# Optimization experiments

Hardware: AMD Instinct MI355X
Metric: run time of the kernel (lower is better)

The kernel has to match this reference:

```python
import jax, jax.numpy as jnp
import numpy as np

B, X, C = 8, 256, 256  # batch, feature axis, topfreq

def setup_inputs() -> dict:
    key = jax.random.key(0)
    k1, k2, k3, k4 = jax.random.split(key, 4)
    return {
        "amplitude": jax.random.normal(k1, (B, X, C), dtype=jnp.float32),
        "phase": jax.random.normal(k2, (B, X, C), dtype=jnp.float32),
        "A": jax.random.normal(k3, (C, C), dtype=jnp.float32),
        "w_amplitude": jnp.asarray(0.5, dtype=jnp.float32),
        "w_phase": jnp.asarray(0.5, dtype=jnp.float32),
        # uniform noise for gumbel sampling; keep away from 0 to avoid -log(-log(0))
        "gumbel_u": jax.random.uniform(k4, (B, C, C, 2), dtype=jnp.float32, minval=1e-6, maxval=1.0),
    }

def reference(amplitude, phase, A, w_amplitude, w_phase, gumbel_u):
    # pairwise diffs: (b, x, c, c)
    a_diff = amplitude[..., :, None] - amplitude[..., None, :]
    p_diff = phase[..., :, None] - phase[..., None, :]
    fused = w_amplitude * a_diff + w_phase * p_diff
    # einsum 'dd,bxcd->bxcd' == multiply by diag(A) along last dim
    temp = jnp.diagonal(A) * fused
    # einsum 'bxcd,bxcd->bcd' == sum of squares over x
    dist = jnp.sum(temp * temp, axis=1)  # (b, c, c)
    exp_dist = 1.0 / (dist + 1e-10)
    eye = jnp.eye(C, dtype=exp_dist.dtype)
    off_diag = 1.0 - eye
    exp_dist = exp_dist * off_diag
    exp_max = jax.lax.stop_gradient(jnp.max(exp_dist, axis=-1, keepdims=True))
    p = exp_dist / exp_max
    p = (p * off_diag + eye) * 0.99  # (b, c, c) in (0, 0.99]
    # bernoulli via 2-class gumbel-softmax (tau=1, hard, straight-through)
    logit = jnp.log(p / (1.0 - p))
    logits = jnp.stack([logit, -logit], axis=-1)  # (b, c, c, 2)
    g = -jnp.log(-jnp.log(gumbel_u))
    y = jax.nn.softmax(logits + g, axis=-1)
    y0 = y[..., 0]
    hard0 = (y0 > y[..., 1]).astype(y.dtype)
    sample = hard0 - jax.lax.stop_gradient(y0) + y0  # straight-through
    mask = sample.mean(axis=0)  # (c, c)
    return mask
```

## Files before the change

kernel.cpp:

```cpp
#include <hip/hip_runtime.h>

#define BB 8
#define XX 256
#define CC 256
#define TCD 8
#define TCE 4
#define TD 4
#define SPLIT 16
#define XH (XX / SPLIT)
#define GX 4



__global__ __launch_bounds__(256) void k_u(
    const float* __restrict__ amp, const float* __restrict__ ph,
    const float* __restrict__ wAp, const float* __restrict__ wPp,
    float* __restrict__ u, float* __restrict__ out)
{
    const float wa = wAp[0], wp = wPp[0];
    const int i = blockIdx.x * 256 + threadIdx.x;
    const float4 a = ((const float4*)amp)[i];
    const float4 p = ((const float4*)ph)[i];
    float4 r;
    r.x = __fadd_rn(__fmul_rn(wa, a.x), __fmul_rn(wp, p.x));
    r.y = __fadd_rn(__fmul_rn(wa, a.y), __fmul_rn(wp, p.y));
    r.z = __fadd_rn(__fmul_rn(wa, a.z), __fmul_rn(wp, p.z));
    r.w = __fadd_rn(__fmul_rn(wa, a.w), __fmul_rn(wp, p.w));
    ((float4*)u)[i] = r;

    if (blockIdx.x < 64) {
        ((float4*)out)[blockIdx.x * 256 + threadIdx.x] = make_float4(0.f, 0.f, 0.f, 0.f);
    }
}

#define ULOAD4(BU, GIDX) {                                        \
    const float* _p = ud_base + (size_t)(GIDX) * GX * CC;         \
    _Pragma("unroll")                                             \
    for (int i = 0; i < GX; ++i)                                  \
        BU[i] = *(const float4*)(_p + (size_t)i * CC);            }

#define UCOMP4(BU, GIDX) {                                        \
    const int _xb = xloc + (GIDX) * GX;                           \
    _Pragma("unroll")                                             \
    for (int i = 0; i < GX; ++i) {                                \
        const float4 ud4 = BU[i];                                 \
        const float4 cA = cols[_xb + i][0];                       \
        const float4 cB = cols[_xb + i][1];                       \
        _Pragma("unroll")                                         \
        for (int k = 0; k < 4; ++k) {                             \
            const float uv = (k==0)?ud4.x:(k==1)?ud4.y:(k==2)?ud4.z:ud4.w; \
            gacc[0][k] = fmaf(cA.x, uv, gacc[0][k]);              \
            gacc[1][k] = fmaf(cA.y, uv, gacc[1][k]);              \
            gacc[2][k] = fmaf(cA.z, uv, gacc[2][k]);              \
            gacc[3][k] = fmaf(cA.w, uv, gacc[3][k]);              \
            gacc[4][k] = fmaf(cB.x, uv, gacc[4][k]);              \
            gacc[5][k] = fmaf(cB.y, uv, gacc[5][k]);              \
            gacc[6][k] = fmaf(cB.z, uv, gacc[6][k]);              \
            gacc[7][k] = fmaf(cB.w, uv, gacc[7][k]);              \
            sacc[k]    = fmaf(uv, uv, sacc[k]);                   \
        }                                                         \
    } }

__global__ __launch_bounds__(256, 4) void k_dist(
    const float* __restrict__ u,
    float* __restrict__ wsd)
{
    const int tid  = threadIdx.x;
    const int lane = tid & 63;
    const int w    = tid >> 6;
    const int c0   = blockIdx.x * TCD;
    const int b    = blockIdx.y;
    const int cz   = blockIdx.z * 4 + w;
    const int x0b  = blockIdx.z * 64;
    const int xloc = w * XH;
    const int d0   = lane * TD;

    __shared__ float4 cols[64][2];
    if (tid < 128) {
        const int x = tid >> 1, h = tid & 1;
        cols[x][h] = *(const float4*)(u + ((size_t)b * XX + x0b + x) * CC + c0 + 4 * h);
    }
    __syncthreads();

    const float* ud_base = u + ((size_t)b * XX + x0b + xloc) * CC + d0;

    float gacc[TCD][4];
#pragma unroll
    for (int j = 0; j < TCD; ++j)
#pragma unroll
        for (int k = 0; k < 4; ++k) gacc[j][k] = 0.0f;
    float sacc[4] = {0.f, 0.f, 0.f, 0.f};

    constexpr int NG = XH / GX;
    {
        float4 b0[GX], b1[GX];
        ULOAD4(b0, 0)
        ULOAD4(b1, 1)
        UCOMP4(b0, 0)
        ULOAD4(b0, 2)
        UCOMP4(b1, 1)
        ULOAD4(b1, 3)
        UCOMP4(b0, 2)
        UCOMP4(b1, 3)
        static_assert(NG == 4, "pipeline hard-coded for NG==4");
    }

    __shared__ float sS[4][CC];
    *(float4*)&sS[w][d0] = make_float4(sacc[0], sacc[1], sacc[2], sacc[3]);
    __syncthreads();

    float* wbase = wsd + (((size_t)cz * BB + b) * CC + c0) * CC + d0;
#pragma unroll
    for (int j = 0; j < TCD; ++j) {
        const float scj = sS[w][c0 + j];
        float4 o;
        o.x = fmaf(-2.0f, gacc[j][0], __fadd_rn(scj, sacc[0]));
        o.y = fmaf(-2.0f, gacc[j][1], __fadd_rn(scj, sacc[1]));
        o.z = fmaf(-2.0f, gacc[j][2], __fadd_rn(scj, sacc[2]));
        o.w = fmaf(-2.0f, gacc[j][3], __fadd_rn(scj, sacc[3]));
        *(float4*)(wbase + (size_t)j * CC) = o;
    }
}

__global__ __launch_bounds__(256, 4) void k_epi(
    const float* __restrict__ wsd, const float* __restrict__ A,
    const float* __restrict__ gu,  float* __restrict__ out)
{
    const int d  = threadIdx.x;
    const int c0 = blockIdx.x * TCE;
    const int b  = blockIdx.y;

    const float dAd  = A[(size_t)d * CC + d];
    const float dAd2 = __fmul_rn(dAd, dAd);

    float pv[TCE][SPLIT];
#pragma unroll
    for (int j = 0; j < TCE; ++j) {
        const size_t ro = ((size_t)b * CC + c0 + j) * CC + d;
#pragma unroll
        for (int h = 0; h < SPLIT; ++h)
            pv[j][h] = wsd[(size_t)h * BB * CC * CC + ro];
    }

    float dist[TCE];
#pragma unroll
    for (int j = 0; j < TCE; ++j) {
        float p = pv[j][0];
#pragma unroll
        for (int h = 1; h < SPLIT; ++h) p = __fadd_rn(p, pv[j][h]);
        dist[j] = __fmul_rn(dAd2, p);
    }

    float ed[TCE];
#pragma unroll
    for (int j = 0; j < TCE; ++j)
        ed[j] = (d == c0 + j) ? 0.0f : __fdiv_rn(1.0f, __fadd_rn(dist[j], 1e-10f));

    __shared__ float wmax[TCE][4];
    const int wave = threadIdx.x >> 6;
    const int lane = threadIdx.x & 63;
#pragma unroll
    for (int j = 0; j < TCE; ++j) {
        float v = ed[j];
#pragma unroll
        for (int m = 1; m < 64; m <<= 1) v = fmaxf(v, __shfl_xor(v, m));
        if (lane == 0) wmax[j][wave] = v;
    }
    __syncthreads();

#pragma unroll
    for (int j = 0; j < TCE; ++j) {
        const int c = c0 + j;
        float em = fmaxf(fmaxf(wmax[j][0], wmax[j][1]), fmaxf(wmax[j][2], wmax[j][3]));
        float p;
        if (d == c) {
            p = 0.99f;
        } else {
            p = __fmul_rn(__fdiv_rn(ed[j], em), 0.99f);
        }
        float logit = logf(__fdiv_rn(p, __fsub_rn(1.0f, p)));

        const float2 g2 = *(const float2*)(gu + (((size_t)b * CC + c) * CC + d) * 2);
        float g0 = -logf(-logf(g2.x));
        float g1 = -logf(-logf(g2.y));

        float a0 = __fadd_rn(logit, g0);
        float a1 = __fadd_rn(-logit, g1);
        float m  = fmaxf(a0, a1);
        float e0 = expf(__fsub_rn(a0, m));
        float e1 = expf(__fsub_rn(a1, m));
        float s  = __fadd_rn(e0, e1);
        float y0 = __fdiv_rn(e0, s);
        float y1 = __fdiv_rn(e1, s);
        if (y0 > y1) {
            atomicAdd(&out[(size_t)c * CC + d], 0.125f);
        }
    }
}


#define STEPU(UC, ACC) {                         \
    float diff = __fsub_rn(UC, ud);              \
    float t    = __fmul_rn(dAd, diff);           \
    float sq   = __fmul_rn(t, t);                \
    ACC = __fadd_rn(ACC, sq);                    \
}

#define LOADG(BA, BP, GIDX) {                    \
    const float* _a = ampbd + (size_t)(GIDX) * 8 * CC; \
    const float* _p = phbd  + (size_t)(GIDX) * 8 * CC; \
    _Pragma("unroll")                            \
    for (int i = 0; i < 8; ++i) {                \
        BA[i] = _a[(size_t)i * CC];              \
        BP[i] = _p[(size_t)i * CC];              \
    }                                            \
}

#define COMPG(BA, BP, GIDX) {                    \
    const int _xb = (GIDX) * 8;                  \
    _Pragma("unroll")                            \
    for (int i = 0; i < 8; ++i) {                \
        const float av = BA[i];                  \
        const float pv = BP[i];                  \
        const float ud = __fadd_rn(__fmul_rn(wa, av), __fmul_rn(wp, pv)); \
        const float4 uc = cols[_xb + i];         \
        STEPU(uc.x, acc0)                        \
        STEPU(uc.y, acc1)                        \
        STEPU(uc.z, acc2)                        \
        STEPU(uc.w, acc3)                        \
    }                                            \
}

__global__ __launch_bounds__(256, 2) void k_fused(
    const float* __restrict__ amp, const float* __restrict__ ph,
    const float* __restrict__ A,   const float* __restrict__ wAp,
    const float* __restrict__ wPp, const float* __restrict__ gu,
    float* __restrict__ out)
{
    const int d  = threadIdx.x;
    const int c0 = blockIdx.x * TCE;
    const int b  = blockIdx.y;

    const float wa = wAp[0];
    const float wp = wPp[0];

    __shared__ float4 cols[XX];
    {
        const int x = threadIdx.x;
        const size_t base = ((size_t)b * XX + x) * CC + c0;
        const float4 a4 = *(const float4*)(amp + base);
        const float4 p4 = *(const float4*)(ph  + base);
        float4 uu;
        uu.x = __fadd_rn(__fmul_rn(wa, a4.x), __fmul_rn(wp, p4.x));
        uu.y = __fadd_rn(__fmul_rn(wa, a4.y), __fmul_rn(wp, p4.y));
        uu.z = __fadd_rn(__fmul_rn(wa, a4.z), __fmul_rn(wp, p4.z));
        uu.w = __fadd_rn(__fmul_rn(wa, a4.w), __fmul_rn(wp, p4.w));
        cols[x] = uu;
    }
    __syncthreads();

    const float dAd = A[(size_t)d * CC + d];
    const float* ampbd = amp + (size_t)b * XX * CC + d;
    const float* phbd  = ph  + (size_t)b * XX * CC + d;

    float acc0 = 0.0f, acc1 = 0.0f, acc2 = 0.0f, acc3 = 0.0f;
    constexpr int NG = XX / 8;
    {
        float b0A[8], b0P[8], b1A[8], b1P[8];
        LOADG(b0A, b0P, 0)
        for (int g = 0; g + 2 < NG; g += 2) {
            LOADG(b1A, b1P, g + 1)
            COMPG(b0A, b0P, g)
            LOADG(b0A, b0P, g + 2)
            COMPG(b1A, b1P, g + 1)
        }
        LOADG(b1A, b1P, NG - 1)
        COMPG(b0A, b0P, NG - 2)
        COMPG(b1A, b1P, NG - 1)
    }

    float ed[TCE];
    ed[0] = (d == c0)     ? 0.0f : __fdiv_rn(1.0f, __fadd_rn(acc0, 1e-10f));
    ed[1] = (d == c0 + 1) ? 0.0f : __fdiv_rn(1.0f, __fadd_rn(acc1, 1e-10f));
    ed[2] = (d == c0 + 2) ? 0.0f : __fdiv_rn(1.0f, __fadd_rn(acc2, 1e-10f));
    ed[3] = (d == c0 + 3) ? 0.0f : __fdiv_rn(1.0f, __fadd_rn(acc3, 1e-10f));

    __shared__ float wmax[TCE][4];
    const int wave = threadIdx.x >> 6;
    const int lane = threadIdx.x & 63;
#pragma unroll
    for (int j = 0; j < TCE; ++j) {
        float v = ed[j];
#pragma unroll
        for (int m = 1; m < 64; m <<= 1) v = fmaxf(v, __shfl_xor(v, m));
        if (lane == 0) wmax[j][wave] = v;
    }
    __syncthreads();

#pragma unroll
    for (int j = 0; j < TCE; ++j) {
        const int c = c0 + j;
        float em = fmaxf(fmaxf(wmax[j][0], wmax[j][1]), fmaxf(wmax[j][2], wmax[j][3]));
        float p;
        if (d == c) {
            p = 0.99f;
        } else {
            p = __fmul_rn(__fdiv_rn(ed[j], em), 0.99f);
        }
        float logit = logf(__fdiv_rn(p, __fsub_rn(1.0f, p)));

        const float2 g2 = *(const float2*)(gu + (((size_t)b * CC + c) * CC + d) * 2);
        float g0 = -logf(-logf(g2.x));
        float g1 = -logf(-logf(g2.y));

        float a0 = __fadd_rn(logit, g0);
        float a1 = __fadd_rn(-logit, g1);
        float m  = fmaxf(a0, a1);
        float e0 = expf(__fsub_rn(a0, m));
        float e1 = expf(__fsub_rn(a1, m));
        float s  = __fadd_rn(e0, e1);
        float y0 = __fdiv_rn(e0, s);
        float y1 = __fdiv_rn(e1, s);
        if (y0 > y1) {
            atomicAdd(&out[(size_t)c * CC + d], 0.125f);
        }
    }
}

extern "C" void kernel_launch(void* const* d_in, const int* in_sizes, int n_in,
                              void* d_out, int out_size, void* d_ws, size_t ws_size,
                              hipStream_t stream) {
    const float* amp = (const float*)d_in[0];
    const float* ph  = (const float*)d_in[1];
    const float* A   = (const float*)d_in[2];
    const float* wa  = (const float*)d_in[3];
    const float* wp  = (const float*)d_in[4];
    const float* gu  = (const float*)d_in[5];
    float* out = (float*)d_out;

    const size_t uElems = (size_t)BB * XX * CC;
    const size_t pElems = (size_t)SPLIT * BB * CC * CC;
    const size_t need = (uElems + pElems) * sizeof(float);
    if (ws_size >= need) {
        float* ud  = (float*)d_ws;
        float* wsd = ud + uElems;
        k_u<<<uElems / 4 / 256, 256, 0, stream>>>(amp, ph, wa, wp, ud, out);
        dim3 g1(CC / TCD, BB, SPLIT / 4);
        k_dist<<<g1, 256, 0, stream>>>(ud, wsd);
        dim3 g2(CC / TCE, BB);
        k_epi<<<g2, 256, 0, stream>>>(wsd, A, gu, out);
    } else {
        hipMemsetAsync(out, 0, (size_t)CC * CC * sizeof(float), stream);
        dim3 g(CC / TCE, BB);
        k_fused<<<g, 256, 0, stream>>>(amp, ph, A, wa, wp, gu, out);
    }
}
```

Measured before the change: 93.83 us.

## Shrink x-split to four partials and use two-column tiles in distance kernel

The distance kernel now tiles two c columns per block instead of eight and splits the x axis into four partial sums instead of sixteen. Each wave covers a 64-row x slice through a looped double-buffered pipeline. This cuts the partial-sum workspace traffic and the epilogue reduction by a factor of four. The cost is less reuse of each loaded u row across columns (two FMAs per element instead of eight) and more total global reads of u.

Result: faster. 89.95 us (-4.1%).

```diff
diff --git a/kernel.cpp b/kernel.cpp
--- a/kernel.cpp
+++ b/kernel.cpp
@@ -3,10 +3,10 @@
 #define BB 8
 #define XX 256
 #define CC 256
-#define TCD 8
+#define TCD 2
 #define TCE 4
 #define TD 4
-#define SPLIT 16
+#define SPLIT 4
 #define XH (XX / SPLIT)
 #define GX 4
 
@@ -33,32 +33,31 @@
     }
 }
 
-#define ULOAD4(BU, GIDX) {                                        \
+
+#define ULOAD(BU, GIDX) {                                         \
     const float* _p = ud_base + (size_t)(GIDX) * GX * CC;         \
     _Pragma("unroll")                                             \
     for (int i = 0; i < GX; ++i)                                  \
         BU[i] = *(const float4*)(_p + (size_t)i * CC);            }
 
-#define UCOMP4(BU, GIDX) {                                        \
+#define UCOMP(BU, GIDX) {                                         \
     const int _xb = xloc + (GIDX) * GX;                           \
     _Pragma("unroll")                                             \
     for (int i = 0; i < GX; ++i) {                                \
         const float4 ud4 = BU[i];                                 \
-        const float4 cA = cols[_xb + i][0];                       \
-        const float4 cB = cols[_xb + i][1];                       \
-        _Pragma("unroll")                                         \
-        for (int k = 0; k < 4; ++k) {                             \
-            const float uv = (k==0)?ud4.x:(k==1)?ud4.y:(k==2)?ud4.z:ud4.w; \
-            gacc[0][k] = fmaf(cA.x, uv, gacc[0][k]);              \
-            gacc[1][k] = fmaf(cA.y, uv, gacc[1][k]);              \
-            gacc[2][k] = fmaf(cA.z, uv, gacc[2][k]);              \
-            gacc[3][k] = fmaf(cA.w, uv, gacc[3][k]);              \
-            gacc[4][k] = fmaf(cB.x, uv, gacc[4][k]);              \
-            gacc[5][k] = fmaf(cB.y, uv, gacc[5][k]);              \
-            gacc[6][k] = fmaf(cB.z, uv, gacc[6][k]);              \
-            gacc[7][k] = fmaf(cB.w, uv, gacc[7][k]);              \
-            sacc[k]    = fmaf(uv, uv, sacc[k]);                   \
-        }                                                         \
+        const float2 cc  = cols[_xb + i];                         \
+        g00 = fmaf(cc.x, ud4.x, g00);                             \
+        g01 = fmaf(cc.x, ud4.y, g01);                             \
+        g02 = fmaf(cc.x, ud4.z, g02);                             \
+        g03 = fmaf(cc.x, ud4.w, g03);                             \
+        g10 = fmaf(cc.y, ud4.x, g10);                             \
+        g11 = fmaf(cc.y, ud4.y, g11);                             \
+        g12 = fmaf(cc.y, ud4.z, g12);                             \
+        g13 = fmaf(cc.y, ud4.w, g13);                             \
+        s0  = fmaf(ud4.x, ud4.x, s0);                             \
+        s1  = fmaf(ud4.y, ud4.y, s1);                             \
+        s2  = fmaf(ud4.z, ud4.z, s2);                             \
+        s3  = fmaf(ud4.w, ud4.w, s3);                             \
     } }
 
 __global__ __launch_bounds__(256, 4) void k_dist(
@@ -70,57 +69,58 @@
     const int w    = tid >> 6;
     const int c0   = blockIdx.x * TCD;
     const int b    = blockIdx.y;
-    const int cz   = blockIdx.z * 4 + w;
-    const int x0b  = blockIdx.z * 64;
     const int xloc = w * XH;
     const int d0   = lane * TD;
 
-    __shared__ float4 cols[64][2];
-    if (tid < 128) {
-        const int x = tid >> 1, h = tid & 1;
-        cols[x][h] = *(const float4*)(u + ((size_t)b * XX + x0b + x) * CC + c0 + 4 * h);
-    }
-    __syncthreads();
-
-    const float* ud_base = u + ((size_t)b * XX + x0b + xloc) * CC + d0;
-
-    float gacc[TCD][4];
-#pragma unroll
-    for (int j = 0; j < TCD; ++j)
-#pragma unroll
-        for (int k = 0; k < 4; ++k) gacc[j][k] = 0.0f;
-    float sacc[4] = {0.f, 0.f, 0.f, 0.f};
+    __shared__ float2 cols[XX];
+    if (tid < XX) {
+        const float* cp = u + ((size_t)b * XX + tid) * CC + c0;
+        cols[tid] = make_float2(cp[0], cp[1]);
+    }
+    __syncthreads();
+
+    const float* ud_base = u + ((size_t)b * XX + xloc) * CC + d0;
+
+    float g00=0.f,g01=0.f,g02=0.f,g03=0.f;
+    float g10=0.f,g11=0.f,g12=0.f,g13=0.f;
+    float s0=0.f,s1=0.f,s2=0.f,s3=0.f;
 
     constexpr int NG = XH / GX;
     {
         float4 b0[GX], b1[GX];
-        ULOAD4(b0, 0)
-        ULOAD4(b1, 1)
-        UCOMP4(b0, 0)
-        ULOAD4(b0, 2)
-        UCOMP4(b1, 1)
-        ULOAD4(b1, 3)
-        UCOMP4(b0, 2)
-        UCOMP4(b1, 3)
-        static_assert(NG == 4, "pipeline hard-coded for NG==4");
+        ULOAD(b0, 0)
+        for (int g = 0; g + 2 < NG; g += 2) {
+            ULOAD(b1, g + 1)
+            UCOMP(b0, g)
+            ULOAD(b0, g + 2)
+            UCOMP(b1, g + 1)
+        }
+        ULOAD(b1, NG - 1)
+        UCOMP(b0, NG - 2)
+        UCOMP(b1, NG - 1)
     }
 
     __shared__ float sS[4][CC];
-    *(float4*)&sS[w][d0] = make_float4(sacc[0], sacc[1], sacc[2], sacc[3]);
-    __syncthreads();
-
-    float* wbase = wsd + (((size_t)cz * BB + b) * CC + c0) * CC + d0;
-#pragma unroll
-    for (int j = 0; j < TCD; ++j) {
-        const float scj = sS[w][c0 + j];
-        float4 o;
-        o.x = fmaf(-2.0f, gacc[j][0], __fadd_rn(scj, sacc[0]));
-        o.y = fmaf(-2.0f, gacc[j][1], __fadd_rn(scj, sacc[1]));
-        o.z = fmaf(-2.0f, gacc[j][2], __fadd_rn(scj, sacc[2]));
-        o.w = fmaf(-2.0f, gacc[j][3], __fadd_rn(scj, sacc[3]));
-        *(float4*)(wbase + (size_t)j * CC) = o;
-    }
-}
+    *(float4*)&sS[w][d0] = make_float4(s0, s1, s2, s3);
+    __syncthreads();
+
+    const float sc0 = sS[w][c0];
+    const float sc1 = sS[w][c0 + 1];
+
+    float* wbase = wsd + (((size_t)w * BB + b) * CC + c0) * CC + d0;
+    float4 o0, o1;
+    o0.x = fmaf(-2.0f, g00, __fadd_rn(sc0, s0));
+    o0.y = fmaf(-2.0f, g01, __fadd_rn(sc0, s1));
+    o0.z = fmaf(-2.0f, g02, __fadd_rn(sc0, s2));
+    o0.w = fmaf(-2.0f, g03, __fadd_rn(sc0, s3));
+    o1.x = fmaf(-2.0f, g10, __fadd_rn(sc1, s0));
+    o1.y = fmaf(-2.0f, g11, __fadd_rn(sc1, s1));
+    o1.z = fmaf(-2.0f, g12, __fadd_rn(sc1, s2));
+    o1.w = fmaf(-2.0f, g13, __fadd_rn(sc1, s3));
+    *(float4*)(wbase)          = o0;
+    *(float4*)(wbase + CC)     = o1;
+}
+
 
 __global__ __launch_bounds__(256, 4) void k_epi(
     const float* __restrict__ wsd, const float* __restrict__ A,
@@ -133,21 +133,14 @@
     const float dAd  = A[(size_t)d * CC + d];
     const float dAd2 = __fmul_rn(dAd, dAd);
 
-    float pv[TCE][SPLIT];
+    float dist[TCE];
 #pragma unroll
     for (int j = 0; j < TCE; ++j) {
         const size_t ro = ((size_t)b * CC + c0 + j) * CC + d;
-#pragma unroll
-        for (int h = 0; h < SPLIT; ++h)
-            pv[j][h] = wsd[(size_t)h * BB * CC * CC + ro];
-    }
-
-    float dist[TCE];
-#pragma unroll
-    for (int j = 0; j < TCE; ++j) {
-        float p = pv[j][0];
-#pragma unroll
-        for (int h = 1; h < SPLIT; ++h) p = __fadd_rn(p, pv[j][h]);
+        float p = wsd[ro];
+#pragma unroll
+        for (int h = 1; h < SPLIT; ++h)
+            p = __fadd_rn(p, wsd[(size_t)h * BB * CC * CC + ro]);
         dist[j] = __fmul_rn(dAd2, p);
     }
 
@@ -345,7 +338,7 @@
         float* ud  = (float*)d_ws;
         float* wsd = ud + uElems;
         k_u<<<uElems / 4 / 256, 256, 0, stream>>>(amp, ph, wa, wp, ud, out);
-        dim3 g1(CC / TCD, BB, SPLIT / 4);
+        dim3 g1(CC / TCD, BB);
         k_dist<<<g1, 256, 0, stream>>>(ud, wsd);
         dim3 g2(CC / TCE, BB);
         k_epi<<<g2, 256, 0, stream>>>(wsd, A, gu, out);
```

## Fuse weighted-sum prep into distance kernel and halve split-K partials

Applied to the files above, without the earlier changes.

Removes the separate k_u kernel by computing u = wa*amp + wp*ph on the fly inside k_dist, which now reads amp and ph directly and zeroes the output itself. The x-split drops from 16 to 8, so each wave accumulates over 32 rows and the partial-distance workspace and epilogue reads are halved. This saves a launch and the u round-trip through memory, at the cost of loading two input arrays per element, recomputing u for every column tile, and running half as many k_dist blocks with a lower occupancy hint.

After: 84.15 us. -10.3%, faster.

```diff
diff --git a/kernel.cpp b/kernel.cpp
--- a/kernel.cpp
+++ b/kernel.cpp
@@ -6,107 +6,114 @@
 #define TCD 8
 #define TCE 4
 #define TD 4
-#define SPLIT 16
-#define XH (XX / SPLIT)
+#define SPLIT 8
+#define XHW 32
 #define GX 4
 
 
 
-__global__ __launch_bounds__(256) void k_u(
-    const float* __restrict__ amp, const float* __restrict__ ph,
-    const float* __restrict__ wAp, const float* __restrict__ wPp,
-    float* __restrict__ u, float* __restrict__ out)
-{
-    const float wa = wAp[0], wp = wPp[0];
-    const int i = blockIdx.x * 256 + threadIdx.x;
-    const float4 a = ((const float4*)amp)[i];
-    const float4 p = ((const float4*)ph)[i];
-    float4 r;
-    r.x = __fadd_rn(__fmul_rn(wa, a.x), __fmul_rn(wp, p.x));
-    r.y = __fadd_rn(__fmul_rn(wa, a.y), __fmul_rn(wp, p.y));
-    r.z = __fadd_rn(__fmul_rn(wa, a.z), __fmul_rn(wp, p.z));
-    r.w = __fadd_rn(__fmul_rn(wa, a.w), __fmul_rn(wp, p.w));
-    ((float4*)u)[i] = r;
-
-    if (blockIdx.x < 64) {
-        ((float4*)out)[blockIdx.x * 256 + threadIdx.x] = make_float4(0.f, 0.f, 0.f, 0.f);
-    }
-}
-
-#define ULOAD4(BU, GIDX) {                                        \
-    const float* _p = ud_base + (size_t)(GIDX) * GX * CC;         \
+#define AULOAD(BA, BP, GIDX) {                                    \
+    const float* _a = ampbd + (size_t)(GIDX) * GX * CC;           \
+    const float* _p = phbd  + (size_t)(GIDX) * GX * CC;           \
     _Pragma("unroll")                                             \
-    for (int i = 0; i < GX; ++i)                                  \
-        BU[i] = *(const float4*)(_p + (size_t)i * CC);            }
-
-#define UCOMP4(BU, GIDX) {                                        \
+    for (int i = 0; i < GX; ++i) {                                \
+        BA[i] = *(const float4*)(_a + (size_t)i * CC);            \
+        BP[i] = *(const float4*)(_p + (size_t)i * CC);            \
+    } }
+
+#define AUCOMP(BA, BP, GIDX) {                                    \
     const int _xb = xloc + (GIDX) * GX;                           \
     _Pragma("unroll")                                             \
     for (int i = 0; i < GX; ++i) {                                \
-        const float4 ud4 = BU[i];                                 \
+        const float4 a4 = BA[i];                                  \
+        const float4 p4 = BP[i];                                  \
+        float4 ud4;                                               \
+        ud4.x = __fadd_rn(__fmul_rn(wa, a4.x), __fmul_rn(wp, p4.x)); \
+        ud4.y = __fadd_rn(__fmul_rn(wa, a4.y), __fmul_rn(wp, p4.y)); \
+        ud4.z = __fadd_rn(__fmul_rn(wa, a4.z), __fmul_rn(wp, p4.z)); \
+        ud4.w = __fadd_rn(__fmul_rn(wa, a4.w), __fmul_rn(wp, p4.w)); \
         const float4 cA = cols[_xb + i][0];                       \
         const float4 cB = cols[_xb + i][1];                       \
         _Pragma("unroll")                                         \
         for (int k = 0; k < 4; ++k) {                             \
             const float uv = (k==0)?ud4.x:(k==1)?ud4.y:(k==2)?ud4.z:ud4.w; \
-            gacc[0][k] = fmaf(cA.x, uv, gacc[0][k]);              \
-            gacc[1][k] = fmaf(cA.y, uv, gacc[1][k]);              \
-            gacc[2][k] = fmaf(cA.z, uv, gacc[2][k]);              \
-            gacc[3][k] = fmaf(cA.w, uv, gacc[3][k]);              \
-            gacc[4][k] = fmaf(cB.x, uv, gacc[4][k]);              \
-            gacc[5][k] = fmaf(cB.y, uv, gacc[5][k]);              \
-            gacc[6][k] = fmaf(cB.z, uv, gacc[6][k]);              \
-            gacc[7][k] = fmaf(cB.w, uv, gacc[7][k]);              \
-            sacc[k]    = fmaf(uv, uv, sacc[k]);                   \
+            g[0][k] = fmaf(cA.x, uv, g[0][k]);                    \
+            g[1][k] = fmaf(cA.y, uv, g[1][k]);                    \
+            g[2][k] = fmaf(cA.z, uv, g[2][k]);                    \
+            g[3][k] = fmaf(cA.w, uv, g[3][k]);                    \
+            g[4][k] = fmaf(cB.x, uv, g[4][k]);                    \
+            g[5][k] = fmaf(cB.y, uv, g[5][k]);                    \
+            g[6][k] = fmaf(cB.z, uv, g[6][k]);                    \
+            g[7][k] = fmaf(cB.w, uv, g[7][k]);                    \
+            s[k]    = fmaf(uv, uv, s[k]);                         \
         }                                                         \
     } }
 
-__global__ __launch_bounds__(256, 4) void k_dist(
-    const float* __restrict__ u,
-    float* __restrict__ wsd)
+__global__ __launch_bounds__(256, 2) void k_dist(
+    const float* __restrict__ amp, const float* __restrict__ ph,
+    const float* __restrict__ wAp, const float* __restrict__ wPp,
+    float* __restrict__ wsd,
+    float* __restrict__ out)
 {
-    const int tid  = threadIdx.x;
-    const int lane = tid & 63;
-    const int w    = tid >> 6;
-    const int c0   = blockIdx.x * TCD;
-    const int b    = blockIdx.y;
-    const int cz   = blockIdx.z * 4 + w;
-    const int x0b  = blockIdx.z * 64;
-    const int xloc = w * XH;
-    const int d0   = lane * TD;
-
-    __shared__ float4 cols[64][2];
-    if (tid < 128) {
+    const int tid   = threadIdx.x;
+    const int lane  = tid & 63;
+    const int w     = tid >> 6;
+    const int c0    = blockIdx.x * TCD;
+    const int b     = blockIdx.y;
+    const int xhalf = blockIdx.z * 128;
+    const int cz    = blockIdx.z * 4 + w;
+    const int xloc  = w * XHW;
+    const int d0    = lane * TD;
+
+    if (blockIdx.y == 0 && blockIdx.z == 0) {
+        ((float4*)out)[blockIdx.x * 512 + tid]       = make_float4(0.f,0.f,0.f,0.f);
+        ((float4*)out)[blockIdx.x * 512 + 256 + tid] = make_float4(0.f,0.f,0.f,0.f);
+    }
+
+    const float wa = wAp[0], wp = wPp[0];
+
+    __shared__ float4 cols[128][2];
+    {
         const int x = tid >> 1, h = tid & 1;
-        cols[x][h] = *(const float4*)(u + ((size_t)b * XX + x0b + x) * CC + c0 + 4 * h);
-    }
-    __syncthreads();
-
-    const float* ud_base = u + ((size_t)b * XX + x0b + xloc) * CC + d0;
-
-    float gacc[TCD][4];
+        const size_t base = ((size_t)b * XX + xhalf + x) * CC + c0 + 4 * h;
+        const float4 a4 = *(const float4*)(amp + base);
+        const float4 p4 = *(const float4*)(ph  + base);
+        float4 uu;
+        uu.x = __fadd_rn(__fmul_rn(wa, a4.x), __fmul_rn(wp, p4.x));
+        uu.y = __fadd_rn(__fmul_rn(wa, a4.y), __fmul_rn(wp, p4.y));
+        uu.z = __fadd_rn(__fmul_rn(wa, a4.z), __fmul_rn(wp, p4.z));
+        uu.w = __fadd_rn(__fmul_rn(wa, a4.w), __fmul_rn(wp, p4.w));
+        cols[x][h] = uu;
+    }
+    __syncthreads();
+
+    const float* ampbd = amp + ((size_t)b * XX + xhalf + xloc) * CC + d0;
+    const float* phbd  = ph  + ((size_t)b * XX + xhalf + xloc) * CC + d0;
+
+    float g[TCD][4];
 #pragma unroll
     for (int j = 0; j < TCD; ++j)
 #pragma unroll
-        for (int k = 0; k < 4; ++k) gacc[j][k] = 0.0f;
-    float sacc[4] = {0.f, 0.f, 0.f, 0.f};
-
-    constexpr int NG = XH / GX;
+        for (int k = 0; k < 4; ++k) g[j][k] = 0.0f;
+    float s[4] = {0.f, 0.f, 0.f, 0.f};
+
+    constexpr int NG = XHW / GX;
     {
-        float4 b0[GX], b1[GX];
-        ULOAD4(b0, 0)
-        ULOAD4(b1, 1)
-        UCOMP4(b0, 0)
-        ULOAD4(b0, 2)
-        UCOMP4(b1, 1)
-        ULOAD4(b1, 3)
-        UCOMP4(b0, 2)
-        UCOMP4(b1, 3)
-        static_assert(NG == 4, "pipeline hard-coded for NG==4");
+        float4 b0A[GX], b0P[GX], b1A[GX], b1P[GX];
+        AULOAD(b0A, b0P, 0)
+        for (int gg = 0; gg + 2 < NG; gg += 2) {
+            AULOAD(b1A, b1P, gg + 1)
+            AUCOMP(b0A, b0P, gg)
+            AULOAD(b0A, b0P, gg + 2)
+            AUCOMP(b1A, b1P, gg + 1)
+        }
+        AULOAD(b1A, b1P, NG - 1)
+        AUCOMP(b0A, b0P, NG - 2)
+        AUCOMP(b1A, b1P, NG - 1)
     }
 
     __shared__ float sS[4][CC];
-    *(float4*)&sS[w][d0] = make_float4(sacc[0], sacc[1], sacc[2], sacc[3]);
+    *(float4*)&sS[w][d0] = make_float4(s[0], s[1], s[2], s[3]);
     __syncthreads();
 
     float* wbase = wsd + (((size_t)cz * BB + b) * CC + c0) * CC + d0;
@@ -114,13 +121,14 @@
     for (int j = 0; j < TCD; ++j) {
         const float scj = sS[w][c0 + j];
         float4 o;
-        o.x = fmaf(-2.0f, gacc[j][0], __fadd_rn(scj, sacc[0]));
-        o.y = fmaf(-2.0f, gacc[j][1], __fadd_rn(scj, sacc[1]));
-        o.z = fmaf(-2.0f, gacc[j][2], __fadd_rn(scj, sacc[2]));
-        o.w = fmaf(-2.0f, gacc[j][3], __fadd_rn(scj, sacc[3]));
+        o.x = fmaf(-2.0f, g[j][0], __fadd_rn(scj, s[0]));
+        o.y = fmaf(-2.0f, g[j][1], __fadd_rn(scj, s[1]));
+        o.z = fmaf(-2.0f, g[j][2], __fadd_rn(scj, s[2]));
+        o.w = fmaf(-2.0f, g[j][3], __fadd_rn(scj, s[3]));
         *(float4*)(wbase + (size_t)j * CC) = o;
     }
 }
+
 
 __global__ __launch_bounds__(256, 4) void k_epi(
     const float* __restrict__ wsd, const float* __restrict__ A,
@@ -133,21 +141,14 @@
     const float dAd  = A[(size_t)d * CC + d];
     const float dAd2 = __fmul_rn(dAd, dAd);
 
-    float pv[TCE][SPLIT];
+    float dist[TCE];
 #pragma unroll
     for (int j = 0; j < TCE; ++j) {
         const size_t ro = ((size_t)b * CC + c0 + j) * CC + d;
-#pragma unroll
-        for (int h = 0; h < SPLIT; ++h)
-            pv[j][h] = wsd[(size_t)h * BB * CC * CC + ro];
-    }
-
-    float dist[TCE];
-#pragma unroll
-    for (int j = 0; j < TCE; ++j) {
-        float p = pv[j][0];
-#pragma unroll
-        for (int h = 1; h < SPLIT; ++h) p = __fadd_rn(p, pv[j][h]);
+        float p = wsd[ro];
+#pragma unroll
+        for (int h = 1; h < SPLIT; ++h)
+            p = __fadd_rn(p, wsd[(size_t)h * BB * CC * CC + ro]);
         dist[j] = __fmul_rn(dAd2, p);
     }
 
@@ -189,9 +190,9 @@
         float m  = fmaxf(a0, a1);
         float e0 = expf(__fsub_rn(a0, m));
         float e1 = expf(__fsub_rn(a1, m));
-        float s  = __fadd_rn(e0, e1);
-        float y0 = __fdiv_rn(e0, s);
-        float y1 = __fdiv_rn(e1, s);
+        float sm = __fadd_rn(e0, e1);
+        float y0 = __fdiv_rn(e0, sm);
+        float y1 = __fdiv_rn(e1, sm);
         if (y0 > y1) {
             atomicAdd(&out[(size_t)c * CC + d], 0.125f);
         }
@@ -318,9 +319,9 @@
         float m  = fmaxf(a0, a1);
         float e0 = expf(__fsub_rn(a0, m));
         float e1 = expf(__fsub_rn(a1, m));
-        float s  = __fadd_rn(e0, e1);
-        float y0 = __fdiv_rn(e0, s);
-        float y1 = __fdiv_rn(e1, s);
+        float sm = __fadd_rn(e0, e1);
+        float y0 = __fdiv_rn(e0, sm);
+        float y1 = __fdiv_rn(e1, sm);
         if (y0 > y1) {
             atomicAdd(&out[(size_t)c * CC + d], 0.125f);
         }
@@ -338,15 +339,12 @@
     const float* gu  = (const float*)d_in[5];
     float* out = (float*)d_out;
 
-    const size_t uElems = (size_t)BB * XX * CC;
     const size_t pElems = (size_t)SPLIT * BB * CC * CC;
-    const size_t need = (uElems + pElems) * sizeof(float);
+    const size_t need = pElems * sizeof(float);
     if (ws_size >= need) {
-        float* ud  = (float*)d_ws;
-        float* wsd = ud + uElems;
-        k_u<<<uElems / 4 / 256, 256, 0, stream>>>(amp, ph, wa, wp, ud, out);
-        dim3 g1(CC / TCD, BB, SPLIT / 4);
-        k_dist<<<g1, 256, 0, stream>>>(ud, wsd);
+        float* wsd = (float*)d_ws;
+        dim3 g1(CC / TCD, BB, 2);
+        k_dist<<<g1, 256, 0, stream>>>(amp, ph, wa, wp, wsd, out);
         dim3 g2(CC / TCE, BB);
         k_epi<<<g2, 256, 0, stream>>>(wsd, A, gu, out);
     } else {
```
